# Kernel tuning notes

Measured on AMD Instinct MI355X. Metric: run time of the kernel, lower is better.

The kernel has to match this reference:

```python
import jax, jax.numpy as jnp
import numpy as np

N = 100000   # nodes
E = 1280000  # edges (avg degree 16)
F = 64       # node_features
H = 64       # hidden_dim
L = 4        # residual GIN layers after conv1 (num_layers-1)
G = 128      # number of graphs in batch
BN_EPS = 1e-5


def setup_inputs() -> dict:
    key = jax.random.key(0)
    ks = jax.random.split(key, 16)
    x = jax.random.normal(ks[0], (N, F), jnp.float32)
    edge_index = jax.random.randint(ks[1], (2, E), 0, N, jnp.int32)
    batch = jnp.sort(jax.random.randint(ks[2], (N,), 0, G, jnp.int32))

    def lin_w(k, fi, fo, *lead):
        return jax.random.normal(k, (*lead, fi, fo), jnp.float32) / np.float32(np.sqrt(fi))

    inp = {"x": x, "edge_index": edge_index, "batch": batch}
    # conv1 MLP: Linear(F,H) ReLU Linear(H,H) ReLU BN(H)
    inp["c1_W1"] = lin_w(ks[3], F, H)
    inp["c1_b1"] = jnp.zeros((H,), jnp.float32)
    inp["c1_W2"] = lin_w(ks[4], H, H)
    inp["c1_b2"] = jnp.zeros((H,), jnp.float32)
    inp["c1_g"] = jnp.ones((H,), jnp.float32)
    inp["c1_be"] = jnp.zeros((H,), jnp.float32)
    inp["c1_m"] = 0.1 * jax.random.normal(ks[5], (H,), jnp.float32)
    inp["c1_v"] = 0.5 + jax.random.uniform(ks[6], (H,), jnp.float32)
    # 4 residual convs, params stacked on leading dim L
    inp["cs_W1"] = lin_w(ks[7], H, H, L)
    inp["cs_b1"] = jnp.zeros((L, H), jnp.float32)
    inp["cs_W2"] = lin_w(ks[8], H, H, L)
    inp["cs_b2"] = jnp.zeros((L, H), jnp.float32)
    inp["cs_g"] = jnp.ones((L, H), jnp.float32)
    inp["cs_be"] = jnp.zeros((L, H), jnp.float32)
    inp["cs_m"] = 0.1 * jax.random.normal(ks[9], (L, H), jnp.float32)
    inp["cs_v"] = 0.5 + jax.random.uniform(ks[10], (L, H), jnp.float32)
    # final Linear+Tanh head
    inp["lin_W"] = lin_w(ks[11], H, H)
    inp["lin_b"] = jnp.zeros((H,), jnp.float32)
    return inp


def _gin_conv(h, src, dst, W1, b1, W2, b2, g, be, m, v):
    # GIN (eps=0): mlp(x + sum_{j in N(i)} x_j); messages flow src->dst
    agg = jax.ops.segment_sum(h[src], dst, num_segments=h.shape[0])
    z = h + agg
    z = jax.nn.relu(z @ W1 + b1)
    z = jax.nn.relu(z @ W2 + b2)
    # BatchNorm1d (eval mode, running stats)
    return (z - m) * jax.lax.rsqrt(v + BN_EPS) * g + be


def reference(x, edge_index, batch, c1_W1, c1_b1, c1_W2, c1_b2, c1_g, c1_be, c1_m, c1_v,
              cs_W1, cs_b1, cs_W2, cs_b2, cs_g, cs_be, cs_m, cs_v, lin_W, lin_b):
    src, dst = edge_index[0], edge_index[1]
    h = _gin_conv(x, src, dst, c1_W1, c1_b1, c1_W2, c1_b2, c1_g, c1_be, c1_m, c1_v)
    for i in range(cs_W1.shape[0]):
        h = h + _gin_conv(h, src, dst, cs_W1[i], cs_b1[i], cs_W2[i], cs_b2[i],
                          cs_g[i], cs_be[i], cs_m[i], cs_v[i])
    out = jnp.tanh(h @ lin_W + lin_b)
    # global_mean_pool over batch ids
    sums = jax.ops.segment_sum(out, batch, num_segments=G)
    cnt = jax.ops.segment_sum(jnp.ones((out.shape[0], 1), out.dtype), batch, num_segments=G)
    return sums / jnp.maximum(cnt, 1.0)
```

## Files before the change

### kernel.cpp

```cpp
#include <hip/hip_runtime.h>
#include <hip/hip_bf16.h>

constexpr int N_NODES  = 100000;
constexpr int N_EDGES  = 1280000;
constexpr int HDIM     = 64;
constexpr int N_GRAPHS = 128;
constexpr int N_RES    = 4;
constexpr int CAP      = 64;
constexpr int ZNODE    = N_NODES;

typedef __attribute__((ext_vector_type(8))) short bf16x8;
typedef __attribute__((ext_vector_type(4))) float f32x4;

__device__ __forceinline__ unsigned f2bf1(float f) {
  unsigned u = __float_as_uint(f);
  return (u + 0x7fffu + ((u >> 16) & 1u)) >> 16;
}
__device__ __forceinline__ unsigned packbf(float lo, float hi) {
  return f2bf1(lo) | (f2bf1(hi) << 16);
}
__device__ __forceinline__ float bflo(unsigned u) { return __uint_as_float(u << 16); }
__device__ __forceinline__ float bfhi(unsigned u) { return __uint_as_float(u & 0xffff0000u); }
__device__ __forceinline__ float bf2f(unsigned short h) { return __uint_as_float(((unsigned)h) << 16); }

__device__ __forceinline__ float tanh_fast(float x) {
  float xc = fminf(fmaxf(x, -15.f), 15.f);
  float e = __expf(2.f * xc);
  return __fdividef(e - 1.f, e + 1.f);
}

constexpr int RNG = 8;
constexpr int RSZ = N_NODES / RNG;
constexpr int CHUNKS = 128;
constexpr int CSZ = N_EDGES / CHUNKS;

__global__ void fill_kernel(const int* __restrict__ ei,
                            int* __restrict__ cnt, int* __restrict__ csr) {
  int b = blockIdx.x;
  int lo = (b & (RNG - 1)) * RSZ;
  int hi = lo + RSZ;
  int base = (b >> 3) * CSZ;
  for (int i = base + threadIdx.x * 4; i < base + CSZ; i += 256 * 4) {
    int4 d4 = *(const int4*)&ei[N_EDGES + i];
    int4 s4 = *(const int4*)&ei[i];
    if (d4.x >= lo && d4.x < hi) { int p = atomicAdd(&cnt[d4.x], 1); csr[d4.x * CAP + (p & (CAP - 1))] = s4.x; }
    if (d4.y >= lo && d4.y < hi) { int p = atomicAdd(&cnt[d4.y], 1); csr[d4.y * CAP + (p & (CAP - 1))] = s4.y; }
    if (d4.z >= lo && d4.z < hi) { int p = atomicAdd(&cnt[d4.z], 1); csr[d4.z * CAP + (p & (CAP - 1))] = s4.z; }
    if (d4.w >= lo && d4.w < hi) { int p = atomicAdd(&cnt[d4.w], 1); csr[d4.w * CAP + (p & (CAP - 1))] = s4.w; }
  }
}

__global__ void prefill_kernel(int* __restrict__ csr) {
  int n = blockIdx.x * blockDim.x + threadIdx.x;
  if (n > N_NODES) return;
  int4 z4 = make_int4(ZNODE, ZNODE, ZNODE, ZNODE);
  int4* p = (int4*)(csr + (size_t)n * CAP);
  p[0] = z4; p[1] = z4; p[2] = z4; p[3] = z4;
}

__global__ void cvt_pad_kernel(const float* __restrict__ x, unsigned short* __restrict__ dst) {
  constexpr int TOT = (N_NODES + 1) * HDIM / 2;
  constexpr int XN  = N_NODES * HDIM / 2;
  unsigned* d = (unsigned*)dst;
  for (int i = blockIdx.x * blockDim.x + threadIdx.x; i < TOT; i += gridDim.x * blockDim.x) {
    unsigned v = 0;
    if (i < XN) { float2 f = *(const float2*)&x[i * 2]; v = packbf(f.x, f.y); }
    d[i] = v;
  }
}

__global__ void goff_kernel(const int* __restrict__ batch, int* __restrict__ goff) {
  int g = threadIdx.x;
  if (g > N_GRAPHS) return;
  int lo = 0, hi = N_NODES;
  while (lo < hi) {
    int mid = (lo + hi) >> 1;
    if (batch[mid] < g) lo = mid + 1; else hi = mid;
  }
  goff[g] = lo;
}

__global__ void packw_kernel(const float* __restrict__ c1W1, const float* __restrict__ c1W2,
                             const float* __restrict__ csW1, const float* __restrict__ csW2,
                             unsigned short* __restrict__ dst) {
  int idx = blockIdx.x * 256 + threadIdx.x;
  if (idx >= 10 * 4096) return;
  int mat = idx >> 12;
  int e   = idx & 4095;
  int f    = e >> 9;
  int lane = (e >> 3) & 63;
  int i    = e & 7;
  int tc = f >> 1, ks = f & 1;
  int krow = ks * 32 + (lane >> 4) * 8 + i;
  int col  = tc * 16 + (lane & 15);
  int l = mat >> 1;
  const float* W;
  if (l == 0) W = (mat & 1) ? c1W2 : c1W1;
  else        W = ((mat & 1) ? csW2 : csW1) + (size_t)(l - 1) * 4096;
  float w = W[krow * 64 + col];
  unsigned short hi = (unsigned short)f2bf1(w);
  unsigned short lo = (unsigned short)f2bf1(w - bf2f(hi));
  unsigned short* d = dst + (size_t)mat * 8192;
  d[e] = hi;
  d[4096 + e] = lo;
}

template <bool RESID>
__global__ __launch_bounds__(256, 6)
void conv_kernel(const unsigned short* __restrict__ hin, unsigned short* __restrict__ hout,
                 const int* __restrict__ cnt, const int* __restrict__ csr,
                 const unsigned short* __restrict__ Wpk,
                 const float* __restrict__ b1, const float* __restrict__ b2,
                 const float* __restrict__ gam, const float* __restrict__ bet,
                 const float* __restrict__ rm, const float* __restrict__ rv) {
  __shared__ __align__(16) unsigned short zb0[64][72];
  __shared__ __align__(16) unsigned short zb1[64][72];
  const int t   = threadIdx.x;
  const int ln  = t & 63;
  const int wid = __builtin_amdgcn_readfirstlane(t >> 6);
  const int lc  = ln & 31;
  const bool hiH = ln >= 32;
  const int nb  = blockIdx.x * 64;
  const unsigned* hb = (const unsigned*)hin;

  for (int p = 0; p < 8; ++p) {
    int m = wid * 16 + 2 * p;
    int nA = nb + m; if (nA > ZNODE) nA = ZNODE;
    int nB = nA + 1; if (nB > ZNODE) nB = ZNODE;
    const int* rA = csr + (size_t)nA * CAP;
    const int* rB = csr + (size_t)nB * CAP;
    int4 a0 = *(const int4*)(rA + 0), a1q = *(const int4*)(rA + 4);
    int4 a2 = *(const int4*)(rA + 8), a3q = *(const int4*)(rA + 12);
    int4 b0 = *(const int4*)(rB + 0), b1q = *(const int4*)(rB + 4);
    int4 b2q = *(const int4*)(rB + 8), b3q = *(const int4*)(rB + 12);
    int dA = cnt[nA], dB = cnt[nB];

    int self = hiH ? nB : nA;
    float z0, z1;
    { unsigned u = hb[(size_t)self * 32 + lc]; z0 = bflo(u); z1 = bfhi(u); }
    int i0  = hiH ? b0.x  : a0.x;   int i1  = hiH ? b0.y  : a0.y;
    int i2  = hiH ? b0.z  : a0.z;   int i3  = hiH ? b0.w  : a0.w;
    int i4  = hiH ? b1q.x : a1q.x;  int i5  = hiH ? b1q.y : a1q.y;
    int i6  = hiH ? b1q.z : a1q.z;  int i7  = hiH ? b1q.w : a1q.w;
    int i8  = hiH ? b2q.x : a2.x;   int i9  = hiH ? b2q.y : a2.y;
    int i10 = hiH ? b2q.z : a2.z;   int i11 = hiH ? b2q.w : a2.w;
    int i12 = hiH ? b3q.x : a3q.x;  int i13 = hiH ? b3q.y : a3q.y;
    int i14 = hiH ? b3q.z : a3q.z;  int i15 = hiH ? b3q.w : a3q.w;
#define GACC(ix) { unsigned u = hb[(size_t)(ix) * 32 + lc]; z0 += bflo(u); z1 += bfhi(u); }
    GACC(i0)  GACC(i1)  GACC(i2)  GACC(i3)
    GACC(i4)  GACC(i5)  GACC(i6)  GACC(i7)
    GACC(i8)  GACC(i9)  GACC(i10) GACC(i11)
    GACC(i12) GACC(i13) GACC(i14) GACC(i15)
#undef GACC
    if (dA > 16 && !hiH)
      for (int q = 16; q < dA; ++q) { unsigned u = hb[(size_t)rA[q] * 32 + lc]; z0 += bflo(u); z1 += bfhi(u); }
    if (dB > 16 && hiH)
      for (int q = 16; q < dB; ++q) { unsigned u = hb[(size_t)rB[q] * 32 + lc]; z0 += bflo(u); z1 += bfhi(u); }
    int mr = m + (hiH ? 1 : 0);
    unsigned h0 = f2bf1(z0);
    float r0 = z0 - __uint_as_float(h0 << 16);
    float r1 = z1 - __uint_as_float(f2bf1(z1) << 16);
    *(unsigned*)&zb0[mr][2 * lc] = h0 | (f2bf1(z1) << 16);
    *(unsigned*)&zb1[mr][2 * lc] = f2bf1(r0) | (f2bf1(r1) << 16);
  }
  __syncthreads();

  const int l15 = ln & 15, lg = ln >> 4;
  const int arow = 16 * wid + l15;
  const unsigned short* W1pk = Wpk;
  const unsigned short* W2pk = Wpk + 8192;

  f32x4 acc[4];
#pragma unroll
  for (int tc = 0; tc < 4; ++tc) {
    float bv = b1[tc * 16 + l15];
    acc[tc] = (f32x4){bv, bv, bv, bv};
  }
#pragma unroll
  for (int ks = 0; ks < 2; ++ks) {
    bf16x8 ah = *(const bf16x8*)&zb0[arow][lg * 8 + ks * 32];
    bf16x8 al = *(const bf16x8*)&zb1[arow][lg * 8 + ks * 32];
#pragma unroll
    for (int tc = 0; tc < 4; ++tc) {
      bf16x8 bh = *(const bf16x8*)&W1pk[(size_t)((tc * 2 + ks) * 64 + ln) * 8];
      bf16x8 bl = *(const bf16x8*)&W1pk[4096 + (size_t)((tc * 2 + ks) * 64 + ln) * 8];
      acc[tc] = __builtin_amdgcn_mfma_f32_16x16x32_bf16(ah, bh, acc[tc], 0, 0, 0);
      acc[tc] = __builtin_amdgcn_mfma_f32_16x16x32_bf16(al, bh, acc[tc], 0, 0, 0);
      acc[tc] = __builtin_amdgcn_mfma_f32_16x16x32_bf16(ah, bl, acc[tc], 0, 0, 0);
    }
  }
  __syncthreads();

#pragma unroll
  for (int tc = 0; tc < 4; ++tc) {
#pragma unroll
    for (int r = 0; r < 4; ++r) {
      float v = fmaxf(acc[tc][r], 0.0f);
      int node = 16 * wid + lg * 4 + r;
      int feat = tc * 16 + l15;
      unsigned short hh = (unsigned short)f2bf1(v);
      zb0[node][feat] = hh;
      zb1[node][feat] = (unsigned short)f2bf1(v - bf2f(hh));
    }
  }
  __syncthreads();

#pragma unroll
  for (int tc = 0; tc < 4; ++tc) {
    float bv = b2[tc * 16 + l15];
    acc[tc] = (f32x4){bv, bv, bv, bv};
  }
#pragma unroll
  for (int ks = 0; ks < 2; ++ks) {
    bf16x8 ah = *(const bf16x8*)&zb0[arow][lg * 8 + ks * 32];
    bf16x8 al = *(const bf16x8*)&zb1[arow][lg * 8 + ks * 32];
#pragma unroll
    for (int tc = 0; tc < 4; ++tc) {
      bf16x8 bh = *(const bf16x8*)&W2pk[(size_t)((tc * 2 + ks) * 64 + ln) * 8];
      bf16x8 bl = *(const bf16x8*)&W2pk[4096 + (size_t)((tc * 2 + ks) * 64 + ln) * 8];
      acc[tc] = __builtin_amdgcn_mfma_f32_16x16x32_bf16(ah, bh, acc[tc], 0, 0, 0);
      acc[tc] = __builtin_amdgcn_mfma_f32_16x16x32_bf16(al, bh, acc[tc], 0, 0, 0);
      acc[tc] = __builtin_amdgcn_mfma_f32_16x16x32_bf16(ah, bl, acc[tc], 0, 0, 0);
    }
  }

#pragma unroll
  for (int tc = 0; tc < 4; ++tc) {
    int feat = tc * 16 + l15;
    float sc = gam[feat] * rsqrtf(rv[feat] + 1e-5f);
    float sh = bet[feat] - rm[feat] * sc;
#pragma unroll
    for (int r = 0; r < 4; ++r) {
      int gn = nb + 16 * wid + lg * 4 + r;
      bool v = gn < N_NODES;
      int gnc = v ? gn : ZNODE;
      float y = fmaxf(acc[tc][r], 0.0f) * sc + sh;
      if (RESID) y += bf2f(hin[(size_t)gnc * 64 + feat]);
      if (v) hout[(size_t)gn * 64 + feat] = (unsigned short)f2bf1(y);
    }
  }
}

__global__ __launch_bounds__(512, 6)
void head_pool_kernel(const unsigned short* __restrict__ hin, float* __restrict__ out,
                      const int* __restrict__ batch,
                      const float* __restrict__ W, const float* __restrict__ b) {
  const int t   = threadIdx.x;
  const int ln  = t & 63;
  const int wid = __builtin_amdgcn_readfirstlane(t >> 6);
  const int n = blockIdx.x * 64 + ln;
  const bool valid = n < N_NODES;
  const int nn = valid ? n : ZNODE;
  const unsigned* hb = (const unsigned*)hin;

  unsigned zp[32];
#pragma unroll
  for (int cc = 0; cc < 8; ++cc) {
    uint4 u = *(const uint4*)&hb[(size_t)nn * 32 + cc * 4];
    zp[cc * 4 + 0] = u.x; zp[cc * 4 + 1] = u.y;
    zp[cc * 4 + 2] = u.z; zp[cc * 4 + 3] = u.w;
  }

  const float* Wp = W + wid * 8;
  const float* bp = b + wid * 8;
  float acc[8];
#pragma unroll
  for (int f = 0; f < 8; ++f) acc[f] = bp[f];
#pragma unroll
  for (int w = 0; w < 32; ++w) {
    float zlo = bflo(zp[w]), zhi = bfhi(zp[w]);
#pragma unroll
    for (int f = 0; f < 8; ++f) acc[f] = fmaf(zlo, Wp[(2 * w) * 64 + f], acc[f]);
#pragma unroll
    for (int f = 0; f < 8; ++f) acc[f] = fmaf(zhi, Wp[(2 * w + 1) * 64 + f], acc[f]);
  }
#pragma unroll
  for (int f = 0; f < 8; ++f) acc[f] = tanh_fast(acc[f]);

  int bg = valid ? batch[n] : -1;
  int gmax = bg;
#pragma unroll
  for (int off = 32; off >= 1; off >>= 1) gmax = max(gmax, __shfl_xor(gmax, off));
  gmax = __builtin_amdgcn_readfirstlane(gmax);
  int g0 = __builtin_amdgcn_readfirstlane(bg);

  for (int g = g0; g <= gmax; ++g) {
    float s[8];
    bool inG = (bg == g);
#pragma unroll
    for (int f = 0; f < 8; ++f) s[f] = inG ? acc[f] : 0.0f;
#pragma unroll
    for (int off = 1; off <= 32; off <<= 1) {
#pragma unroll
      for (int f = 0; f < 8; ++f) s[f] += __shfl_xor(s[f], off);
    }
    float sv = s[0];
    sv = (ln == 1) ? s[1] : sv;  sv = (ln == 2) ? s[2] : sv;
    sv = (ln == 3) ? s[3] : sv;  sv = (ln == 4) ? s[4] : sv;
    sv = (ln == 5) ? s[5] : sv;  sv = (ln == 6) ? s[6] : sv;
    sv = (ln == 7) ? s[7] : sv;
    if (ln < 8) atomicAdd(&out[g * 64 + wid * 8 + ln], sv);
  }
}

__global__ void div_kernel(float* __restrict__ out, const int* __restrict__ goff) {
  int i = blockIdx.x * blockDim.x + threadIdx.x;
  if (i >= N_GRAPHS * 64) return;
  int g = i >> 6;
  int c = goff[g + 1] - goff[g];
  out[i] /= (float)max(c, 1);
}

extern "C" void kernel_launch(void* const* d_in, const int* in_sizes, int n_in,
                              void* d_out, int out_size, void* d_ws, size_t ws_size,
                              hipStream_t stream) {
  const float* x     = (const float*)d_in[0];
  const int*   ei    = (const int*)d_in[1];
  const int*   batch = (const int*)d_in[2];
  const float* c1_W1 = (const float*)d_in[3];
  const float* c1_b1 = (const float*)d_in[4];
  const float* c1_W2 = (const float*)d_in[5];
  const float* c1_b2 = (const float*)d_in[6];
  const float* c1_g  = (const float*)d_in[7];
  const float* c1_be = (const float*)d_in[8];
  const float* c1_m  = (const float*)d_in[9];
  const float* c1_v  = (const float*)d_in[10];
  const float* cs_W1 = (const float*)d_in[11];
  const float* cs_b1 = (const float*)d_in[12];
  const float* cs_W2 = (const float*)d_in[13];
  const float* cs_b2 = (const float*)d_in[14];
  const float* cs_g  = (const float*)d_in[15];
  const float* cs_be = (const float*)d_in[16];
  const float* cs_m  = (const float*)d_in[17];
  const float* cs_v  = (const float*)d_in[18];
  const float* lin_W = (const float*)d_in[19];
  const float* lin_b = (const float*)d_in[20];
  float* out = (float*)d_out;

  size_t cur = 0;
  auto take = [&](size_t bytes) -> void* {
    void* p = (char*)d_ws + cur;
    cur += (bytes + 255) & ~(size_t)255;
    return p;
  };
  int* cnt  = (int*)take((N_NODES + 1) * sizeof(int));
  size_t zbytes = cur;
  int* goff = (int*)take((N_GRAPHS + 1) * sizeof(int));
  int* csr  = (int*)take((size_t)(N_NODES + 1) * CAP * sizeof(int));
  unsigned short* bufA = (unsigned short*)take((size_t)(N_NODES + 1) * HDIM * sizeof(unsigned short));
  unsigned short* bufB = (unsigned short*)take((size_t)(N_NODES + 1) * HDIM * sizeof(unsigned short));
  unsigned short* wpk  = (unsigned short*)take((size_t)10 * 8192 * sizeof(unsigned short));
  (void)ws_size; (void)in_sizes; (void)n_in; (void)out_size;

  hipMemsetAsync(cnt, 0, zbytes, stream);
  hipMemsetAsync(bufA + (size_t)ZNODE * HDIM, 0, HDIM * sizeof(unsigned short), stream);
  hipMemsetAsync(out, 0, N_GRAPHS * 64 * sizeof(float), stream);

  prefill_kernel<<<(N_NODES + 256) / 256, 256, 0, stream>>>(csr);
  fill_kernel<<<RNG * CHUNKS, 256, 0, stream>>>(ei, cnt, csr);
  cvt_pad_kernel<<<2048, 256, 0, stream>>>(x, bufB);
  goff_kernel<<<1, 256, 0, stream>>>(batch, goff);
  packw_kernel<<<160, 256, 0, stream>>>(c1_W1, c1_W2, cs_W1, cs_W2, wpk);

  const int NBLK = (N_NODES + 63) / 64;

  conv_kernel<false><<<NBLK, 256, 0, stream>>>(bufB, bufA, cnt, csr,
      wpk, c1_b1, c1_b2, c1_g, c1_be, c1_m, c1_v);

  unsigned short* srcp = bufA;
  unsigned short* dstp = bufB;
  for (int l = 0; l < N_RES; ++l) {
    conv_kernel<true><<<NBLK, 256, 0, stream>>>(srcp, dstp, cnt, csr,
        wpk + (size_t)(l + 1) * 16384,
        cs_b1 + l * 64, cs_b2 + l * 64,
        cs_g + l * 64, cs_be + l * 64, cs_m + l * 64, cs_v + l * 64);
    unsigned short* tmp = srcp; srcp = dstp; dstp = tmp;
  }
  head_pool_kernel<<<NBLK, 512, 0, stream>>>(srcp, out, batch, lin_W, lin_b);
  div_kernel<<<(N_GRAPHS * 64 + 255) / 256, 256, 0, stream>>>(out, goff);
}
```

Measured before the change: 293.9 us.

## Software-pipeline neighbor gathers in conv kernel and batch atomics in CSR fill

The conv kernel's aggregation loop now double-buffers gathered neighbor rows. It issues the 17 loads for the next node pair before accumulating the current pair, so more memory requests are in flight. Launch bounds drop from 6 to 4 waves per SIMD to give room for the extra registers this needs. The CSR fill kernel now handles 8 edges per thread and issues all its atomics before the dependent stores. The costs are fewer resident waves and possible register pressure or spills.

```diff
diff --git a/kernel.cpp b/kernel.cpp
--- a/kernel.cpp
+++ b/kernel.cpp
@@ -40,13 +40,25 @@
   int lo = (b & (RNG - 1)) * RSZ;
   int hi = lo + RSZ;
   int base = (b >> 3) * CSZ;
-  for (int i = base + threadIdx.x * 4; i < base + CSZ; i += 256 * 4) {
-    int4 d4 = *(const int4*)&ei[N_EDGES + i];
-    int4 s4 = *(const int4*)&ei[i];
-    if (d4.x >= lo && d4.x < hi) { int p = atomicAdd(&cnt[d4.x], 1); csr[d4.x * CAP + (p & (CAP - 1))] = s4.x; }
-    if (d4.y >= lo && d4.y < hi) { int p = atomicAdd(&cnt[d4.y], 1); csr[d4.y * CAP + (p & (CAP - 1))] = s4.y; }
-    if (d4.z >= lo && d4.z < hi) { int p = atomicAdd(&cnt[d4.z], 1); csr[d4.z * CAP + (p & (CAP - 1))] = s4.z; }
-    if (d4.w >= lo && d4.w < hi) { int p = atomicAdd(&cnt[d4.w], 1); csr[d4.w * CAP + (p & (CAP - 1))] = s4.w; }
+  for (int i = base + threadIdx.x * 8; i < base + CSZ; i += 256 * 8) {
+    int4 dq0 = *(const int4*)&ei[N_EDGES + i];
+    int4 dq1 = *(const int4*)&ei[N_EDGES + i + 4];
+    int4 sq0 = *(const int4*)&ei[i];
+    int4 sq1 = *(const int4*)&ei[i + 4];
+    int d[8] = {dq0.x, dq0.y, dq0.z, dq0.w, dq1.x, dq1.y, dq1.z, dq1.w};
+    int s[8] = {sq0.x, sq0.y, sq0.z, sq0.w, sq1.x, sq1.y, sq1.z, sq1.w};
+    int p[8];
+    bool m[8];
+#pragma unroll
+    for (int q = 0; q < 8; ++q) {
+      m[q] = (d[q] >= lo && d[q] < hi);
+      p[q] = 0;
+      if (m[q]) p[q] = atomicAdd(&cnt[d[q]], 1);
+    }
+#pragma unroll
+    for (int q = 0; q < 8; ++q) {
+      if (m[q]) csr[d[q] * CAP + (p[q] & (CAP - 1))] = s[q];
+    }
   }
 }
 
@@ -106,7 +118,7 @@
 }
 
 template <bool RESID>
-__global__ __launch_bounds__(256, 6)
+__global__ __launch_bounds__(256, 4)
 void conv_kernel(const unsigned short* __restrict__ hin, unsigned short* __restrict__ hout,
                  const int* __restrict__ cnt, const int* __restrict__ csr,
                  const unsigned short* __restrict__ Wpk,
@@ -123,7 +135,7 @@
   const int nb  = blockIdx.x * 64;
   const unsigned* hb = (const unsigned*)hin;
 
-  for (int p = 0; p < 8; ++p) {
+  auto issue = [&](int p, unsigned* v, int& onA, int& onB, int& odA, int& odB) {
     int m = wid * 16 + 2 * p;
     int nA = nb + m; if (nA > ZNODE) nA = ZNODE;
     int nB = nA + 1; if (nB > ZNODE) nB = ZNODE;
@@ -133,11 +145,9 @@
     int4 a2 = *(const int4*)(rA + 8), a3q = *(const int4*)(rA + 12);
     int4 b0 = *(const int4*)(rB + 0), b1q = *(const int4*)(rB + 4);
     int4 b2q = *(const int4*)(rB + 8), b3q = *(const int4*)(rB + 12);
-    int dA = cnt[nA], dB = cnt[nB];
-
+    odA = cnt[nA]; odB = cnt[nB];
     int self = hiH ? nB : nA;
-    float z0, z1;
-    { unsigned u = hb[(size_t)self * 32 + lc]; z0 = bflo(u); z1 = bfhi(u); }
+    v[16] = hb[(size_t)self * 32 + lc];
     int i0  = hiH ? b0.x  : a0.x;   int i1  = hiH ? b0.y  : a0.y;
     int i2  = hiH ? b0.z  : a0.z;   int i3  = hiH ? b0.w  : a0.w;
     int i4  = hiH ? b1q.x : a1q.x;  int i5  = hiH ? b1q.y : a1q.y;
@@ -146,22 +156,49 @@
     int i10 = hiH ? b2q.z : a2.z;   int i11 = hiH ? b2q.w : a2.w;
     int i12 = hiH ? b3q.x : a3q.x;  int i13 = hiH ? b3q.y : a3q.y;
     int i14 = hiH ? b3q.z : a3q.z;  int i15 = hiH ? b3q.w : a3q.w;
-#define GACC(ix) { unsigned u = hb[(size_t)(ix) * 32 + lc]; z0 += bflo(u); z1 += bfhi(u); }
-    GACC(i0)  GACC(i1)  GACC(i2)  GACC(i3)
-    GACC(i4)  GACC(i5)  GACC(i6)  GACC(i7)
-    GACC(i8)  GACC(i9)  GACC(i10) GACC(i11)
-    GACC(i12) GACC(i13) GACC(i14) GACC(i15)
-#undef GACC
-    if (dA > 16 && !hiH)
-      for (int q = 16; q < dA; ++q) { unsigned u = hb[(size_t)rA[q] * 32 + lc]; z0 += bflo(u); z1 += bfhi(u); }
-    if (dB > 16 && hiH)
-      for (int q = 16; q < dB; ++q) { unsigned u = hb[(size_t)rB[q] * 32 + lc]; z0 += bflo(u); z1 += bfhi(u); }
-    int mr = m + (hiH ? 1 : 0);
+    v[0]  = hb[(size_t)i0  * 32 + lc];  v[1]  = hb[(size_t)i1  * 32 + lc];
+    v[2]  = hb[(size_t)i2  * 32 + lc];  v[3]  = hb[(size_t)i3  * 32 + lc];
+    v[4]  = hb[(size_t)i4  * 32 + lc];  v[5]  = hb[(size_t)i5  * 32 + lc];
+    v[6]  = hb[(size_t)i6  * 32 + lc];  v[7]  = hb[(size_t)i7  * 32 + lc];
+    v[8]  = hb[(size_t)i8  * 32 + lc];  v[9]  = hb[(size_t)i9  * 32 + lc];
+    v[10] = hb[(size_t)i10 * 32 + lc];  v[11] = hb[(size_t)i11 * 32 + lc];
+    v[12] = hb[(size_t)i12 * 32 + lc];  v[13] = hb[(size_t)i13 * 32 + lc];
+    v[14] = hb[(size_t)i14 * 32 + lc];  v[15] = hb[(size_t)i15 * 32 + lc];
+    onA = nA; onB = nB;
+  };
+
+  auto consume = [&](int p, const unsigned* v, int nA, int nB, int dA, int dB) {
+    float z0 = bflo(v[16]), z1 = bfhi(v[16]);
+#pragma unroll
+    for (int q = 0; q < 16; ++q) { z0 += bflo(v[q]); z1 += bfhi(v[q]); }
+    int dS = hiH ? dB : dA;
+    if (dS > 16) {
+      const int* rS = csr + (size_t)(hiH ? nB : nA) * CAP;
+      for (int q = 16; q < dS; ++q) {
+        unsigned u = hb[(size_t)rS[q] * 32 + lc];
+        z0 += bflo(u); z1 += bfhi(u);
+      }
+    }
+    int mr = wid * 16 + 2 * p + (hiH ? 1 : 0);
     unsigned h0 = f2bf1(z0);
     float r0 = z0 - __uint_as_float(h0 << 16);
     float r1 = z1 - __uint_as_float(f2bf1(z1) << 16);
     *(unsigned*)&zb0[mr][2 * lc] = h0 | (f2bf1(z1) << 16);
     *(unsigned*)&zb1[mr][2 * lc] = f2bf1(r0) | (f2bf1(r1) << 16);
+  };
+
+  unsigned vbufA[17], vbufB[17];
+  int nA0, nB0, dA0, dB0, nA1, nB1, dA1, dB1;
+  issue(0, vbufA, nA0, nB0, dA0, dB0);
+#pragma unroll
+  for (int p = 0; p < 8; ++p) {
+    if (p & 1) {
+      if (p < 7) issue(p + 1, vbufA, nA0, nB0, dA0, dB0);
+      consume(p, vbufB, nA1, nB1, dA1, dB1);
+    } else {
+      if (p < 7) issue(p + 1, vbufB, nA1, nB1, dA1, dB1);
+      consume(p, vbufA, nA0, nB0, dA0, dB0);
+    }
   }
   __syncthreads();
 
```

Result: slower. 342.1 us (+16.4%).

## Merge setup kernels into one prep kernel and batch four-node gathers

Applied to the files above, without the earlier changes.

Four small setup kernels (CSR prefill, x conversion, graph offsets, weight packing) become a single launch, which cuts launch overhead. In conv_kernel each wave now handles two node pairs per iteration and issues all 34 gather loads before any accumulation. This puts more memory loads in flight to hide gather latency, at the cost of more registers and possibly lower occupancy under the launch bound of 6.

```diff
diff --git a/kernel.cpp b/kernel.cpp
--- a/kernel.cpp
+++ b/kernel.cpp
@@ -50,59 +50,58 @@
   }
 }
 
-__global__ void prefill_kernel(int* __restrict__ csr) {
-  int n = blockIdx.x * blockDim.x + threadIdx.x;
-  if (n > N_NODES) return;
-  int4 z4 = make_int4(ZNODE, ZNODE, ZNODE, ZNODE);
-  int4* p = (int4*)(csr + (size_t)n * CAP);
-  p[0] = z4; p[1] = z4; p[2] = z4; p[3] = z4;
-}
-
-__global__ void cvt_pad_kernel(const float* __restrict__ x, unsigned short* __restrict__ dst) {
+__global__ void prep_kernel(const float* __restrict__ x, unsigned short* __restrict__ dstx,
+                            int* __restrict__ csr,
+                            const int* __restrict__ batch, int* __restrict__ goff,
+                            const float* __restrict__ c1W1, const float* __restrict__ c1W2,
+                            const float* __restrict__ csW1, const float* __restrict__ csW2,
+                            unsigned short* __restrict__ wpk) {
+  int i = blockIdx.x * 256 + threadIdx.x;
+
   constexpr int TOT = (N_NODES + 1) * HDIM / 2;
   constexpr int XN  = N_NODES * HDIM / 2;
-  unsigned* d = (unsigned*)dst;
-  for (int i = blockIdx.x * blockDim.x + threadIdx.x; i < TOT; i += gridDim.x * blockDim.x) {
+  unsigned* d = (unsigned*)dstx;
+  for (int k = i; k < TOT; k += 2048 * 256) {
     unsigned v = 0;
-    if (i < XN) { float2 f = *(const float2*)&x[i * 2]; v = packbf(f.x, f.y); }
-    d[i] = v;
-  }
-}
-
-__global__ void goff_kernel(const int* __restrict__ batch, int* __restrict__ goff) {
-  int g = threadIdx.x;
-  if (g > N_GRAPHS) return;
-  int lo = 0, hi = N_NODES;
-  while (lo < hi) {
-    int mid = (lo + hi) >> 1;
-    if (batch[mid] < g) lo = mid + 1; else hi = mid;
-  }
-  goff[g] = lo;
-}
-
-__global__ void packw_kernel(const float* __restrict__ c1W1, const float* __restrict__ c1W2,
-                             const float* __restrict__ csW1, const float* __restrict__ csW2,
-                             unsigned short* __restrict__ dst) {
-  int idx = blockIdx.x * 256 + threadIdx.x;
-  if (idx >= 10 * 4096) return;
-  int mat = idx >> 12;
-  int e   = idx & 4095;
-  int f    = e >> 9;
-  int lane = (e >> 3) & 63;
-  int i    = e & 7;
-  int tc = f >> 1, ks = f & 1;
-  int krow = ks * 32 + (lane >> 4) * 8 + i;
-  int col  = tc * 16 + (lane & 15);
-  int l = mat >> 1;
-  const float* W;
-  if (l == 0) W = (mat & 1) ? c1W2 : c1W1;
-  else        W = ((mat & 1) ? csW2 : csW1) + (size_t)(l - 1) * 4096;
-  float w = W[krow * 64 + col];
-  unsigned short hi = (unsigned short)f2bf1(w);
-  unsigned short lo = (unsigned short)f2bf1(w - bf2f(hi));
-  unsigned short* d = dst + (size_t)mat * 8192;
-  d[e] = hi;
-  d[4096 + e] = lo;
+    if (k < XN) { float2 f = *(const float2*)&x[k * 2]; v = packbf(f.x, f.y); }
+    d[k] = v;
+  }
+
+  if (i <= N_NODES) {
+    int4 z4 = make_int4(ZNODE, ZNODE, ZNODE, ZNODE);
+    int4* p = (int4*)(csr + (size_t)i * CAP);
+    p[0] = z4; p[1] = z4; p[2] = z4; p[3] = z4;
+  }
+
+  if (i < 10 * 4096) {
+    int mat = i >> 12;
+    int e   = i & 4095;
+    int f    = e >> 9;
+    int lane = (e >> 3) & 63;
+    int ii   = e & 7;
+    int tc = f >> 1, ks = f & 1;
+    int krow = ks * 32 + (lane >> 4) * 8 + ii;
+    int col  = tc * 16 + (lane & 15);
+    int l = mat >> 1;
+    const float* W;
+    if (l == 0) W = (mat & 1) ? c1W2 : c1W1;
+    else        W = ((mat & 1) ? csW2 : csW1) + (size_t)(l - 1) * 4096;
+    float w = W[krow * 64 + col];
+    unsigned short hi = (unsigned short)f2bf1(w);
+    unsigned short lo = (unsigned short)f2bf1(w - bf2f(hi));
+    unsigned short* dd = wpk + (size_t)mat * 8192;
+    dd[e] = hi;
+    dd[4096 + e] = lo;
+  }
+
+  if (i <= N_GRAPHS) {
+    int lo = 0, hi = N_NODES;
+    while (lo < hi) {
+      int mid = (lo + hi) >> 1;
+      if (batch[mid] < i) lo = mid + 1; else hi = mid;
+    }
+    goff[i] = lo;
+  }
 }
 
 template <bool RESID>
@@ -123,45 +122,77 @@
   const int nb  = blockIdx.x * 64;
   const unsigned* hb = (const unsigned*)hin;
 
-  for (int p = 0; p < 8; ++p) {
-    int m = wid * 16 + 2 * p;
-    int nA = nb + m; if (nA > ZNODE) nA = ZNODE;
-    int nB = nA + 1; if (nB > ZNODE) nB = ZNODE;
-    const int* rA = csr + (size_t)nA * CAP;
-    const int* rB = csr + (size_t)nB * CAP;
-    int4 a0 = *(const int4*)(rA + 0), a1q = *(const int4*)(rA + 4);
-    int4 a2 = *(const int4*)(rA + 8), a3q = *(const int4*)(rA + 12);
-    int4 b0 = *(const int4*)(rB + 0), b1q = *(const int4*)(rB + 4);
-    int4 b2q = *(const int4*)(rB + 8), b3q = *(const int4*)(rB + 12);
-    int dA = cnt[nA], dB = cnt[nB];
-
-    int self = hiH ? nB : nA;
-    float z0, z1;
-    { unsigned u = hb[(size_t)self * 32 + lc]; z0 = bflo(u); z1 = bfhi(u); }
-    int i0  = hiH ? b0.x  : a0.x;   int i1  = hiH ? b0.y  : a0.y;
-    int i2  = hiH ? b0.z  : a0.z;   int i3  = hiH ? b0.w  : a0.w;
-    int i4  = hiH ? b1q.x : a1q.x;  int i5  = hiH ? b1q.y : a1q.y;
-    int i6  = hiH ? b1q.z : a1q.z;  int i7  = hiH ? b1q.w : a1q.w;
-    int i8  = hiH ? b2q.x : a2.x;   int i9  = hiH ? b2q.y : a2.y;
-    int i10 = hiH ? b2q.z : a2.z;   int i11 = hiH ? b2q.w : a2.w;
-    int i12 = hiH ? b3q.x : a3q.x;  int i13 = hiH ? b3q.y : a3q.y;
-    int i14 = hiH ? b3q.z : a3q.z;  int i15 = hiH ? b3q.w : a3q.w;
-#define GACC(ix) { unsigned u = hb[(size_t)(ix) * 32 + lc]; z0 += bflo(u); z1 += bfhi(u); }
-    GACC(i0)  GACC(i1)  GACC(i2)  GACC(i3)
-    GACC(i4)  GACC(i5)  GACC(i6)  GACC(i7)
-    GACC(i8)  GACC(i9)  GACC(i10) GACC(i11)
-    GACC(i12) GACC(i13) GACC(i14) GACC(i15)
-#undef GACC
-    if (dA > 16 && !hiH)
-      for (int q = 16; q < dA; ++q) { unsigned u = hb[(size_t)rA[q] * 32 + lc]; z0 += bflo(u); z1 += bfhi(u); }
-    if (dB > 16 && hiH)
-      for (int q = 16; q < dB; ++q) { unsigned u = hb[(size_t)rB[q] * 32 + lc]; z0 += bflo(u); z1 += bfhi(u); }
-    int mr = m + (hiH ? 1 : 0);
+  for (int pp = 0; pp < 4; ++pp) {
+    int m = wid * 16 + 4 * pp;
+    int nA0 = nb + m;     if (nA0 > ZNODE) nA0 = ZNODE;
+    int nB0 = nA0 + 1;    if (nB0 > ZNODE) nB0 = ZNODE;
+    int nA1 = nb + m + 2; if (nA1 > ZNODE) nA1 = ZNODE;
+    int nB1 = nA1 + 1;    if (nB1 > ZNODE) nB1 = ZNODE;
+    const int* rA0 = csr + (size_t)nA0 * CAP;
+    const int* rB0 = csr + (size_t)nB0 * CAP;
+    const int* rA1 = csr + (size_t)nA1 * CAP;
+    const int* rB1 = csr + (size_t)nB1 * CAP;
+    int4 a0 = *(const int4*)(rA0 + 0), a1q = *(const int4*)(rA0 + 4);
+    int4 a2 = *(const int4*)(rA0 + 8), a3q = *(const int4*)(rA0 + 12);
+    int4 b0 = *(const int4*)(rB0 + 0), b1q = *(const int4*)(rB0 + 4);
+    int4 b2q = *(const int4*)(rB0 + 8), b3q = *(const int4*)(rB0 + 12);
+    int4 c0 = *(const int4*)(rA1 + 0), c1q = *(const int4*)(rA1 + 4);
+    int4 c2 = *(const int4*)(rA1 + 8), c3q = *(const int4*)(rA1 + 12);
+    int4 e0 = *(const int4*)(rB1 + 0), e1q = *(const int4*)(rB1 + 4);
+    int4 e2 = *(const int4*)(rB1 + 8), e3q = *(const int4*)(rB1 + 12);
+    int dA0c = cnt[nA0], dB0c = cnt[nB0], dA1c = cnt[nA1], dB1c = cnt[nB1];
+
+    int s0 = hiH ? nB0 : nA0;
+    int s1 = hiH ? nB1 : nA1;
+    int ia[16] = {
+      hiH ? b0.x  : a0.x,  hiH ? b0.y  : a0.y,  hiH ? b0.z  : a0.z,  hiH ? b0.w  : a0.w,
+      hiH ? b1q.x : a1q.x, hiH ? b1q.y : a1q.y, hiH ? b1q.z : a1q.z, hiH ? b1q.w : a1q.w,
+      hiH ? b2q.x : a2.x,  hiH ? b2q.y : a2.y,  hiH ? b2q.z : a2.z,  hiH ? b2q.w : a2.w,
+      hiH ? b3q.x : a3q.x, hiH ? b3q.y : a3q.y, hiH ? b3q.z : a3q.z, hiH ? b3q.w : a3q.w };
+    int ja[16] = {
+      hiH ? e0.x  : c0.x,  hiH ? e0.y  : c0.y,  hiH ? e0.z  : c0.z,  hiH ? e0.w  : c0.w,
+      hiH ? e1q.x : c1q.x, hiH ? e1q.y : c1q.y, hiH ? e1q.z : c1q.z, hiH ? e1q.w : c1q.w,
+      hiH ? e2.x  : c2.x,  hiH ? e2.y  : c2.y,  hiH ? e2.z  : c2.z,  hiH ? e2.w  : c2.w,
+      hiH ? e3q.x : c3q.x, hiH ? e3q.y : c3q.y, hiH ? e3q.z : c3q.z, hiH ? e3q.w : c3q.w };
+
+    unsigned v[17], w[17];
+    v[16] = hb[(size_t)s0 * 32 + lc];
+    w[16] = hb[(size_t)s1 * 32 + lc];
+#pragma unroll
+    for (int q = 0; q < 16; ++q) v[q] = hb[(size_t)ia[q] * 32 + lc];
+#pragma unroll
+    for (int q = 0; q < 16; ++q) w[q] = hb[(size_t)ja[q] * 32 + lc];
+
+    float z0 = bflo(v[16]), z1 = bfhi(v[16]);
+#pragma unroll
+    for (int q = 0; q < 16; ++q) { z0 += bflo(v[q]); z1 += bfhi(v[q]); }
+    float y0 = bflo(w[16]), y1 = bfhi(w[16]);
+#pragma unroll
+    for (int q = 0; q < 16; ++q) { y0 += bflo(w[q]); y1 += bfhi(w[q]); }
+
+    int dS0 = hiH ? dB0c : dA0c;
+    if (dS0 > 16) {
+      const int* rS = hiH ? rB0 : rA0;
+      for (int q = 16; q < dS0; ++q) { unsigned u = hb[(size_t)rS[q] * 32 + lc]; z0 += bflo(u); z1 += bfhi(u); }
+    }
+    int dS1 = hiH ? dB1c : dA1c;
+    if (dS1 > 16) {
+      const int* rS = hiH ? rB1 : rA1;
+      for (int q = 16; q < dS1; ++q) { unsigned u = hb[(size_t)rS[q] * 32 + lc]; y0 += bflo(u); y1 += bfhi(u); }
+    }
+
+    int mr0 = m + (hiH ? 1 : 0);
+    int mr1 = m + 2 + (hiH ? 1 : 0);
     unsigned h0 = f2bf1(z0);
     float r0 = z0 - __uint_as_float(h0 << 16);
     float r1 = z1 - __uint_as_float(f2bf1(z1) << 16);
-    *(unsigned*)&zb0[mr][2 * lc] = h0 | (f2bf1(z1) << 16);
-    *(unsigned*)&zb1[mr][2 * lc] = f2bf1(r0) | (f2bf1(r1) << 16);
+    *(unsigned*)&zb0[mr0][2 * lc] = h0 | (f2bf1(z1) << 16);
+    *(unsigned*)&zb1[mr0][2 * lc] = f2bf1(r0) | (f2bf1(r1) << 16);
+    unsigned g0 = f2bf1(y0);
+    float q0 = y0 - __uint_as_float(g0 << 16);
+    float q1 = y1 - __uint_as_float(f2bf1(y1) << 16);
+    *(unsigned*)&zb0[mr1][2 * lc] = g0 | (f2bf1(y1) << 16);
+    *(unsigned*)&zb1[mr1][2 * lc] = f2bf1(q0) | (f2bf1(q1) << 16);
   }
   __syncthreads();
 
@@ -356,11 +387,9 @@
   hipMemsetAsync(bufA + (size_t)ZNODE * HDIM, 0, HDIM * sizeof(unsigned short), stream);
   hipMemsetAsync(out, 0, N_GRAPHS * 64 * sizeof(float), stream);
 
-  prefill_kernel<<<(N_NODES + 256) / 256, 256, 0, stream>>>(csr);
+  prep_kernel<<<2048, 256, 0, stream>>>(x, bufB, csr, batch, goff,
+                                        c1_W1, c1_W2, cs_W1, cs_W2, wpk);
   fill_kernel<<<RNG * CHUNKS, 256, 0, stream>>>(ei, cnt, csr);
-  cvt_pad_kernel<<<2048, 256, 0, stream>>>(x, bufB);
-  goff_kernel<<<1, 256, 0, stream>>>(batch, goff);
-  packw_kernel<<<160, 256, 0, stream>>>(c1_W1, c1_W2, cs_W1, cs_W2, wpk);
 
   const int NBLK = (N_NODES + 63) / 64;
 
```

New measurement: 336.2 us. 14.4% more time.

## Fuse setup kernels into one prep kernel and shrink conv blocks to 16 nodes

Applied to the files above, without the earlier changes.

Merges the four setup kernels (csr prefill, x conversion, goff search, weight packing) into a single prep launch to cut launch overhead. The conv kernel now uses 128-thread blocks that each handle 16 nodes instead of 256 threads and 64 nodes. This raises the block count and occupancy and shrinks shared memory per block. In exchange, both waves compute the full 16-row MFMA tile and each keeps only its half, which doubles MFMA work and weight loads per node.

```diff
diff --git a/kernel.cpp b/kernel.cpp
--- a/kernel.cpp
+++ b/kernel.cpp
@@ -50,81 +50,80 @@
   }
 }
 
-__global__ void prefill_kernel(int* __restrict__ csr) {
-  int n = blockIdx.x * blockDim.x + threadIdx.x;
-  if (n > N_NODES) return;
-  int4 z4 = make_int4(ZNODE, ZNODE, ZNODE, ZNODE);
-  int4* p = (int4*)(csr + (size_t)n * CAP);
-  p[0] = z4; p[1] = z4; p[2] = z4; p[3] = z4;
-}
-
-__global__ void cvt_pad_kernel(const float* __restrict__ x, unsigned short* __restrict__ dst) {
+__global__ void prep_kernel(const float* __restrict__ x, unsigned short* __restrict__ dstx,
+                            int* __restrict__ csr,
+                            const int* __restrict__ batch, int* __restrict__ goff,
+                            const float* __restrict__ c1W1, const float* __restrict__ c1W2,
+                            const float* __restrict__ csW1, const float* __restrict__ csW2,
+                            unsigned short* __restrict__ wpk) {
+  int i = blockIdx.x * 256 + threadIdx.x;
+
   constexpr int TOT = (N_NODES + 1) * HDIM / 2;
   constexpr int XN  = N_NODES * HDIM / 2;
-  unsigned* d = (unsigned*)dst;
-  for (int i = blockIdx.x * blockDim.x + threadIdx.x; i < TOT; i += gridDim.x * blockDim.x) {
+  unsigned* d = (unsigned*)dstx;
+  for (int k = i; k < TOT; k += 2048 * 256) {
     unsigned v = 0;
-    if (i < XN) { float2 f = *(const float2*)&x[i * 2]; v = packbf(f.x, f.y); }
-    d[i] = v;
-  }
-}
-
-__global__ void goff_kernel(const int* __restrict__ batch, int* __restrict__ goff) {
-  int g = threadIdx.x;
-  if (g > N_GRAPHS) return;
-  int lo = 0, hi = N_NODES;
-  while (lo < hi) {
-    int mid = (lo + hi) >> 1;
-    if (batch[mid] < g) lo = mid + 1; else hi = mid;
-  }
-  goff[g] = lo;
-}
-
-__global__ void packw_kernel(const float* __restrict__ c1W1, const float* __restrict__ c1W2,
-                             const float* __restrict__ csW1, const float* __restrict__ csW2,
-                             unsigned short* __restrict__ dst) {
-  int idx = blockIdx.x * 256 + threadIdx.x;
-  if (idx >= 10 * 4096) return;
-  int mat = idx >> 12;
-  int e   = idx & 4095;
-  int f    = e >> 9;
-  int lane = (e >> 3) & 63;
-  int i    = e & 7;
-  int tc = f >> 1, ks = f & 1;
-  int krow = ks * 32 + (lane >> 4) * 8 + i;
-  int col  = tc * 16 + (lane & 15);
-  int l = mat >> 1;
-  const float* W;
-  if (l == 0) W = (mat & 1) ? c1W2 : c1W1;
-  else        W = ((mat & 1) ? csW2 : csW1) + (size_t)(l - 1) * 4096;
-  float w = W[krow * 64 + col];
-  unsigned short hi = (unsigned short)f2bf1(w);
-  unsigned short lo = (unsigned short)f2bf1(w - bf2f(hi));
-  unsigned short* d = dst + (size_t)mat * 8192;
-  d[e] = hi;
-  d[4096 + e] = lo;
+    if (k < XN) { float2 f = *(const float2*)&x[k * 2]; v = packbf(f.x, f.y); }
+    d[k] = v;
+  }
+
+  if (i <= N_NODES) {
+    int4 z4 = make_int4(ZNODE, ZNODE, ZNODE, ZNODE);
+    int4* p = (int4*)(csr + (size_t)i * CAP);
+    p[0] = z4; p[1] = z4; p[2] = z4; p[3] = z4;
+  }
+
+  if (i < 10 * 4096) {
+    int mat = i >> 12;
+    int e   = i & 4095;
+    int f    = e >> 9;
+    int lane = (e >> 3) & 63;
+    int ii   = e & 7;
+    int tc = f >> 1, ks = f & 1;
+    int krow = ks * 32 + (lane >> 4) * 8 + ii;
+    int col  = tc * 16 + (lane & 15);
+    int l = mat >> 1;
+    const float* W;
+    if (l == 0) W = (mat & 1) ? c1W2 : c1W1;
+    else        W = ((mat & 1) ? csW2 : csW1) + (size_t)(l - 1) * 4096;
+    float w = W[krow * 64 + col];
+    unsigned short hi = (unsigned short)f2bf1(w);
+    unsigned short lo = (unsigned short)f2bf1(w - bf2f(hi));
+    unsigned short* dd = wpk + (size_t)mat * 8192;
+    dd[e] = hi;
+    dd[4096 + e] = lo;
+  }
+
+  if (i <= N_GRAPHS) {
+    int lo = 0, hi = N_NODES;
+    while (lo < hi) {
+      int mid = (lo + hi) >> 1;
+      if (batch[mid] < i) lo = mid + 1; else hi = mid;
+    }
+    goff[i] = lo;
+  }
 }
 
 template <bool RESID>
-__global__ __launch_bounds__(256, 6)
+__global__ __launch_bounds__(128, 8)
 void conv_kernel(const unsigned short* __restrict__ hin, unsigned short* __restrict__ hout,
                  const int* __restrict__ cnt, const int* __restrict__ csr,
                  const unsigned short* __restrict__ Wpk,
                  const float* __restrict__ b1, const float* __restrict__ b2,
                  const float* __restrict__ gam, const float* __restrict__ bet,
                  const float* __restrict__ rm, const float* __restrict__ rv) {
-  __shared__ __align__(16) unsigned short zb0[64][72];
-  __shared__ __align__(16) unsigned short zb1[64][72];
+  __shared__ __align__(16) unsigned short zb0[16][72];
+  __shared__ __align__(16) unsigned short zb1[16][72];
   const int t   = threadIdx.x;
   const int ln  = t & 63;
   const int wid = __builtin_amdgcn_readfirstlane(t >> 6);
   const int lc  = ln & 31;
   const bool hiH = ln >= 32;
-  const int nb  = blockIdx.x * 64;
+  const int nb  = blockIdx.x * 16;
   const unsigned* hb = (const unsigned*)hin;
 
-  for (int p = 0; p < 8; ++p) {
-    int m = wid * 16 + 2 * p;
+  for (int p = 0; p < 4; ++p) {
+    int m = wid * 8 + 2 * p;
     int nA = nb + m; if (nA > ZNODE) nA = ZNODE;
     int nB = nA + 1; if (nB > ZNODE) nB = ZNODE;
     const int* rA = csr + (size_t)nA * CAP;
@@ -166,7 +165,7 @@
   __syncthreads();
 
   const int l15 = ln & 15, lg = ln >> 4;
-  const int arow = 16 * wid + l15;
+  const int arow = l15;
   const unsigned short* W1pk = Wpk;
   const unsigned short* W2pk = Wpk + 8192;
 
@@ -195,12 +194,14 @@
   for (int tc = 0; tc < 4; ++tc) {
 #pragma unroll
     for (int r = 0; r < 4; ++r) {
-      float v = fmaxf(acc[tc][r], 0.0f);
-      int node = 16 * wid + lg * 4 + r;
-      int feat = tc * 16 + l15;
-      unsigned short hh = (unsigned short)f2bf1(v);
-      zb0[node][feat] = hh;
-      zb1[node][feat] = (unsigned short)f2bf1(v - bf2f(hh));
+      int node = lg * 4 + r;
+      if ((node >> 3) == wid) {
+        float v = fmaxf(acc[tc][r], 0.0f);
+        int feat = tc * 16 + l15;
+        unsigned short hh = (unsigned short)f2bf1(v);
+        zb0[node][feat] = hh;
+        zb1[node][feat] = (unsigned short)f2bf1(v - bf2f(hh));
+      }
     }
   }
   __syncthreads();
@@ -231,9 +232,10 @@
     float sh = bet[feat] - rm[feat] * sc;
 #pragma unroll
     for (int r = 0; r < 4; ++r) {
-      int gn = nb + 16 * wid + lg * 4 + r;
-      bool v = gn < N_NODES;
-      int gnc = v ? gn : ZNODE;
+      int node = lg * 4 + r;
+      int gn = nb + node;
+      bool v = ((node >> 3) == wid) && (gn < N_NODES);
+      int gnc = (gn < N_NODES) ? gn : ZNODE;
       float y = fmaxf(acc[tc][r], 0.0f) * sc + sh;
       if (RESID) y += bf2f(hin[(size_t)gnc * 64 + feat]);
       if (v) hout[(size_t)gn * 64 + feat] = (unsigned short)f2bf1(y);
@@ -356,26 +358,24 @@
   hipMemsetAsync(bufA + (size_t)ZNODE * HDIM, 0, HDIM * sizeof(unsigned short), stream);
   hipMemsetAsync(out, 0, N_GRAPHS * 64 * sizeof(float), stream);
 
-  prefill_kernel<<<(N_NODES + 256) / 256, 256, 0, stream>>>(csr);
+  prep_kernel<<<2048, 256, 0, stream>>>(x, bufB, csr, batch, goff,
+                                        c1_W1, c1_W2, cs_W1, cs_W2, wpk);
   fill_kernel<<<RNG * CHUNKS, 256, 0, stream>>>(ei, cnt, csr);
-  cvt_pad_kernel<<<2048, 256, 0, stream>>>(x, bufB);
-  goff_kernel<<<1, 256, 0, stream>>>(batch, goff);
-  packw_kernel<<<160, 256, 0, stream>>>(c1_W1, c1_W2, cs_W1, cs_W2, wpk);
-
-  const int NBLK = (N_NODES + 63) / 64;
-
-  conv_kernel<false><<<NBLK, 256, 0, stream>>>(bufB, bufA, cnt, csr,
+
+  const int NBLK = N_NODES / 16;
+
+  conv_kernel<false><<<NBLK, 128, 0, stream>>>(bufB, bufA, cnt, csr,
       wpk, c1_b1, c1_b2, c1_g, c1_be, c1_m, c1_v);
 
   unsigned short* srcp = bufA;
   unsigned short* dstp = bufB;
   for (int l = 0; l < N_RES; ++l) {
-    conv_kernel<true><<<NBLK, 256, 0, stream>>>(srcp, dstp, cnt, csr,
+    conv_kernel<true><<<NBLK, 128, 0, stream>>>(srcp, dstp, cnt, csr,
         wpk + (size_t)(l + 1) * 16384,
         cs_b1 + l * 64, cs_b2 + l * 64,
         cs_g + l * 64, cs_be + l * 64, cs_m + l * 64, cs_v + l * 64);
     unsigned short* tmp = srcp; srcp = dstp; dstp = tmp;
   }
-  head_pool_kernel<<<NBLK, 512, 0, stream>>>(srcp, out, batch, lin_W, lin_b);
+  head_pool_kernel<<<(N_NODES + 63) / 64, 512, 0, stream>>>(srcp, out, batch, lin_W, lin_b);
   div_kernel<<<(N_GRAPHS * 64 + 255) / 256, 256, 0, stream>>>(out, goff);
 }
```

Result: slower. 327.6 us (+11.5%).
